# Kernel optimization log

Hardware: AMD Instinct MI355X
Metric: run time of the kernel (lower is better)

The kernel has to match this reference:

```python
import jax, jax.numpy as jnp
import numpy as np
from jax import lax

B, T, D, H, L = 16, 256, 128, 128, 4  # batch, seq, input_size, hidden, num_layers
NUM_CLASSES = 10
EPS = 1e-5


def instancenorm(x):
    # x: [B, T, C]; InstanceNorm1d normalizes over the length dim (T) per (B, C),
    # biased variance, eps=1e-5, no affine.
    m = x.mean(axis=1, keepdims=True)
    v = x.var(axis=1, keepdims=True)
    return (x - m) / jnp.sqrt(v + EPS)


def lstm_stack(x, Wih, Whh, bih, bhh):
    # x: [B, T, I]; Wih/Whh: [L, 4H, I_or_H]; bih/bhh: [L, 4H]. Gate order i,f,g,o.
    batch = x.shape[0]
    hid = Whh.shape[-1]
    out = x
    for l in range(Wih.shape[0]):
        wih, whh, b = Wih[l], Whh[l], bih[l] + bhh[l]
        h0 = jnp.zeros((batch, hid), dtype=x.dtype)
        c0 = jnp.zeros((batch, hid), dtype=x.dtype)
        xs = out.swapaxes(0, 1)  # [T, B, I]

        def step(carry, xt):
            h, c = carry
            g = xt @ wih.T + h @ whh.T + b
            i, f, gg, o = jnp.split(g, 4, axis=-1)
            c_new = jax.nn.sigmoid(f) * c + jax.nn.sigmoid(i) * jnp.tanh(gg)
            h_new = jax.nn.sigmoid(o) * jnp.tanh(c_new)
            return (h_new, c_new), h_new

        _, hs = lax.scan(step, (h0, c0), xs)
        out = hs.swapaxes(0, 1)  # [B, T, H]
    return out


def setup_inputs() -> dict:
    key = jax.random.key(0)
    ks = jax.random.split(key, 16)
    s = 1.0 / np.sqrt(H)
    u = lambda k, shape: jax.random.uniform(k, shape, jnp.float32, -s, s)
    return {
        "x": jax.random.normal(ks[0], (B, T, D), jnp.float32),
        "Wih": u(ks[1], (L, 4 * H, D)),   # input_size == hidden_size so shapes stack
        "Whh": u(ks[2], (L, 4 * H, H)),
        "bih": u(ks[3], (L, 4 * H)),
        "bhh": u(ks[4], (L, 4 * H)),
        "proj_h_w": u(ks[5], (H, H)),
        "proj_h_b": u(ks[6], (H,)),
        "proj_x_w": u(ks[7], (H, D)),
        "proj_x_b": u(ks[8], (H,)),
        "attn_w": u(ks[9], (H,)),
        "fc_w": u(ks[10], (NUM_CLASSES, H)),
        "fc_b": u(ks[11], (NUM_CLASSES,)),
    }


def reference(x, Wih, Whh, bih, bhh, proj_h_w, proj_h_b, proj_x_w, proj_x_b, attn_w, fc_w, fc_b):
    batch, seq_len, input_dim = x.shape
    # normalize(): means/stdev are detached; torch std is unbiased (ddof=1)
    means = lax.stop_gradient(x.mean(axis=(0, 1), keepdims=True))
    stdev = lax.stop_gradient(x.std(axis=(0, 1), ddof=1, keepdims=True) + EPS)
    x = (x - means) / stdev
    x = instancenorm(x)

    lstm_out = lstm_stack(x, Wih, Whh, bih, bhh)   # dropout is identity in eval
    lstm_out = instancenorm(lstm_out)

    ph = lstm_out @ proj_h_w.T + proj_h_b           # [B, T, H]
    px = x @ proj_x_w.T + proj_x_b                  # [B, T, H]
    px = instancenorm(px)

    # additive attention over expanded [B, T, D, H] (values identical across D,
    # matching the original broadcast/expand semantics)
    combined = jnp.tanh(
        jnp.broadcast_to((ph + px)[:, :, None, :], (batch, seq_len, input_dim, ph.shape[-1]))
    )
    logits = jnp.einsum("btdh,h->btd", combined, attn_w)       # [B, T, D]
    alpha = jax.nn.softmax(logits.reshape(batch, -1), axis=1)   # softmax over T*D
    attention_map = alpha.reshape(batch, seq_len, input_dim)

    # classify: context = sum over (T, D) of lstm_out_ex * alpha
    context = jnp.einsum("bth,btd->bh", ph, attention_map)      # [B, H]
    out = context @ fc_w.T + fc_b                               # [B, num_classes]
    return out, attention_map
```

## Files before the change

### kernel.cpp

```cpp
#include <hip/hip_runtime.h>
#include <math.h>
#include <cstddef>

#define B_ 16
#define T_ 256
#define D_ 128
#define H_ 128
#define L_ 4
#define G_ 512
#define NC_ 10
#define EPS_ 1e-5f
#define C_ 16
#define NCHUNK_ (T_ / C_)

#define HROW_ 144
#define HOFF(k) ((k) + (((k) >> 5) << 2))

typedef float f4v __attribute__((ext_vector_type(4)));

#define LOAD_W8(w, base)                                                   \
    asm volatile(                                                          \
        "global_load_dwordx4 %0, %8, off\n\t"                             \
        "global_load_dwordx4 %1, %8, off offset:16\n\t"                   \
        "global_load_dwordx4 %2, %8, off offset:32\n\t"                   \
        "global_load_dwordx4 %3, %8, off offset:48\n\t"                   \
        "global_load_dwordx4 %4, %8, off offset:64\n\t"                   \
        "global_load_dwordx4 %5, %8, off offset:80\n\t"                   \
        "global_load_dwordx4 %6, %8, off offset:96\n\t"                   \
        "global_load_dwordx4 %7, %8, off offset:112\n\t"                  \
        "s_waitcnt vmcnt(0)"                                               \
        : "=&v"(w[0]), "=&v"(w[1]), "=&v"(w[2]), "=&v"(w[3]),              \
          "=&v"(w[4]), "=&v"(w[5]), "=&v"(w[6]), "=&v"(w[7])               \
        : "v"(base)                                                        \
        : "memory")

#define DOT32R(dst_, warr_, hvarr_)                                        \
    {                                                                      \
        float d0_ = 0.f, d1_ = 0.f;                                        \
        _Pragma("unroll")                                                  \
        for (int j_ = 0; j_ < 8; j_++) {                                   \
            d0_ = fmaf(warr_[j_].x, hvarr_[j_].x, d0_);                    \
            d1_ = fmaf(warr_[j_].y, hvarr_[j_].y, d1_);                    \
            d0_ = fmaf(warr_[j_].z, hvarr_[j_].z, d0_);                    \
            d1_ = fmaf(warr_[j_].w, hvarr_[j_].w, d1_);                    \
        }                                                                  \
        dst_ = d0_ + d1_;                                                  \
    }

__device__ __forceinline__ float sigmoid_(float x) {
    x = fminf(fmaxf(x, -30.f), 30.f);
    return 1.f / (1.f + __expf(-x));
}
__device__ __forceinline__ float tanh_(float x) {
    float ax = fminf(fabsf(x), 15.f);
    float e = __expf(2.f * ax);
    float t = 1.f - 2.f / (e + 1.f);
    return copysignf(t, x);
}
__device__ __forceinline__ void wait_ge_(int* p, int v) {
    if (__hip_atomic_load(p, __ATOMIC_RELAXED, __HIP_MEMORY_SCOPE_AGENT) < v) {
        do { __builtin_amdgcn_s_sleep(1); }
        while (__hip_atomic_load(p, __ATOMIC_RELAXED, __HIP_MEMORY_SCOPE_AGENT) < v);
    }
    (void)__hip_atomic_load(p, __ATOMIC_ACQUIRE, __HIP_MEMORY_SCOPE_AGENT);
}
__device__ __forceinline__ void ast_(float* p, float v) {
    __hip_atomic_store(p, v, __ATOMIC_RELAXED, __HIP_MEMORY_SCOPE_AGENT);
}
__device__ __forceinline__ float ald_(const float* p) {
    return __hip_atomic_load(p, __ATOMIC_RELAXED, __HIP_MEMORY_SCOPE_AGENT);
}

__global__ __launch_bounds__(512) void stats_bd(const float* __restrict__ x,
                                                float* __restrict__ psum,
                                                float* __restrict__ psq) {
    int blk = blockIdx.x;
    int b = blk >> 4, strip = blk & 15;
    int tid = threadIdx.x;
    int d = tid & 127, r = tid >> 7;
    const float* xb = x + (size_t)b * T_ * D_ + (size_t)strip * 16 * D_;
    float s = 0.f, q = 0.f;
    for (int t = r; t < 16; t += 4) {
        float v = xb[t * D_ + d];
        s += v; q += v * v;
    }
    __shared__ float ls[512], lq[512];
    ls[tid] = s; lq[tid] = q;
    __syncthreads();
    if (r == 0) {
        s = ls[d] + ls[d + 128] + ls[d + 256] + ls[d + 384];
        q = lq[d] + lq[d + 128] + lq[d + 256] + lq[d + 384];
        psum[blk * 128 + d] = s;
        psq[blk * 128 + d] = q;
    }
}

__global__ __launch_bounds__(128) void stats_norm(const float* __restrict__ psum,
                                                  const float* __restrict__ psq,
                                                  float* __restrict__ mu_bd,
                                                  float* __restrict__ invn) {
    int d = threadIdx.x;
    float S = 0.f, Q = 0.f;
    float sb[16], qb[16];
    for (int b = 0; b < 16; b++) {
        float s = 0.f, q = 0.f;
        for (int st = 0; st < 16; st++) {
            s += psum[(b * 16 + st) * 128 + d];
            q += psq[(b * 16 + st) * 128 + d];
        }
        sb[b] = s; qb[b] = q; S += s; Q += q;
    }
    float n = (float)(B_ * T_);
    float m = S / n;
    float varu = (Q - n * m * m) / (n - 1.f);
    float sd = sqrtf(fmaxf(varu, 0.f)) + EPS_;
    for (int b = 0; b < 16; b++) {
        float mu = sb[b] * (1.f / T_);
        float varT = qb[b] * (1.f / T_) - mu * mu;
        mu_bd[b * 128 + d] = mu;
        invn[b * 128 + d] = rsqrtf(fmaxf(varT, 0.f) + EPS_ * sd * sd);
    }
}

__global__ __attribute__((amdgpu_waves_per_eu(2, 2))) __launch_bounds__(512)
void megascan(const float* __restrict__ x,
              const float* __restrict__ Wih, const float* __restrict__ Whh,
              const float* __restrict__ bih, const float* __restrict__ bhh,
              const float* __restrict__ proj_x_w, const float* __restrict__ proj_x_b,
              const float* __restrict__ proj_h_w, const float* __restrict__ proj_h_b,
              const float* __restrict__ attn_w,
              const float* __restrict__ fc_w, const float* __restrict__ fc_b,
              const float* __restrict__ mu_bd, const float* __restrict__ invn,
              float* __restrict__ h_glob,
              float* __restrict__ ring,
              float* __restrict__ px,
              float* __restrict__ mu_px, float* __restrict__ inv_px,
              float* __restrict__ mu_ln, float* __restrict__ inv_ln,
              float* __restrict__ lsc,
              float* __restrict__ out, float* __restrict__ out_att,
              int* __restrict__ flag_h,
              int* __restrict__ flag_g,
              int* __restrict__ flag_px,
              int* __restrict__ flag_ln,
              int* __restrict__ cnt) {
    const int wg = blockIdx.x;
    const int tid = threadIdx.x;
    __shared__ __align__(16) float shbuf[16 * HROW_];
    __shared__ __align__(16) float sAs[64][32];
    __shared__ __align__(16) float sBs[32][132];
    __shared__ float sred[64][33];
    __shared__ float stmp[256], swsh[256], sctx[512];

    if (wg < 64) {
        const int r = tid >> 2, q = tid & 3;
        const int l = wg >> 4, b = wg & 15;
        f4v w0[8], w1[8], w2[8], w3[8];
        const float* wl = Whh + (size_t)l * G_ * 128;
        LOAD_W8(w0, wl + ((size_t)(0 * 128 + r)) * 128 + q * 32);
        LOAD_W8(w1, wl + ((size_t)(1 * 128 + r)) * 128 + q * 32);
        LOAD_W8(w2, wl + ((size_t)(2 * 128 + r)) * 128 + q * 32);
        LOAD_W8(w3, wl + ((size_t)(3 * 128 + r)) * 128 + q * 32);
        float c = 0.f;
        if (tid < HROW_) shbuf[tid] = 0.f;
        const float* rsl = ring + ((size_t)l * 16 + b) * (4 * C_ * G_);
        float* hob = h_glob + ((size_t)l * 16 + b) * T_ * 128;
        int* fg = flag_g + l * 16 + b;
        int* fh = flag_h + l * 16 + b;
        float hreg[C_];
        __syncthreads();

        for (int k = 0; k < NCHUNK_; k++) {
            if (tid == 0) wait_ge_(fg, k + 1);
            __syncthreads();
#pragma unroll
            for (int half = 0; half < 2; half++) {
                float p0[8], p1[8], p2[8], p3[8];
#pragma unroll
                for (int s8 = 0; s8 < 8; s8++) {
                    int s = half * 8 + s8;
                    const float* gp = rsl + ((size_t)(k & 3) * C_ + s) * G_;
                    p0[s8] = ald_(gp + r);
                    p1[s8] = ald_(gp + 128 + r);
                    p2[s8] = ald_(gp + 256 + r);
                    p3[s8] = ald_(gp + 384 + r);
                }
#pragma unroll
                for (int s8 = 0; s8 < 8; s8++) {
                    int s = half * 8 + s8;
                    int t = k * C_ + s;
                    const f4v* hb4 = (const f4v*)(shbuf + (t & 1) * HROW_ + q * 36);
                    f4v hv[8];
#pragma unroll
                    for (int j = 0; j < 8; j++) hv[j] = hb4[j];
                    float zi, zf, zg, zo;
                    DOT32R(zi, w0, hv);
                    DOT32R(zf, w1, hv);
                    DOT32R(zg, w2, hv);
                    DOT32R(zo, w3, hv);
                    zi += __shfl_xor(zi, 1); zi += __shfl_xor(zi, 2);
                    zf += __shfl_xor(zf, 1); zf += __shfl_xor(zf, 2);
                    zg += __shfl_xor(zg, 1); zg += __shfl_xor(zg, 2);
                    zo += __shfl_xor(zo, 1); zo += __shfl_xor(zo, 2);
                    zi += p0[s8]; zf += p1[s8]; zg += p2[s8]; zo += p3[s8];
                    float ai = sigmoid_(zi), af = sigmoid_(zf);
                    float ag = tanh_(zg),    ao = sigmoid_(zo);
                    c = fmaf(af, c, ai * ag);
                    float hn = ao * tanh_(c);
                    if (q == 0) shbuf[((t + 1) & 1) * HROW_ + HOFF(r)] = hn;
                    hreg[s] = hn;
                    __syncthreads();
                }
            }
            if (q == 0) {
#pragma unroll
                for (int s = 0; s < C_; s++)
                    ast_(hob + (size_t)(k * C_ + s) * 128 + r, hreg[s]);
            }
            __syncthreads();
            if (tid == 0) __hip_atomic_store(fh, k + 1, __ATOMIC_RELEASE, __HIP_MEMORY_SCOPE_AGENT);
        }
    } else if (wg < 128) {
        const int r = tid >> 2, q = tid & 3;
        const int l = (wg - 64) >> 4, b = (wg - 64) & 15;
        f4v w0[8], w1[8], w2[8], w3[8];
        const float* wl = Wih + (size_t)l * G_ * 128;
        LOAD_W8(w0, wl + ((size_t)(0 * 128 + r)) * 128 + q * 32);
        LOAD_W8(w1, wl + ((size_t)(1 * 128 + r)) * 128 + q * 32);
        LOAD_W8(w2, wl + ((size_t)(2 * 128 + r)) * 128 + q * 32);
        LOAD_W8(w3, wl + ((size_t)(3 * 128 + r)) * 128 + q * 32);
        float bs0 = bih[l * G_ + r] + bhh[l * G_ + r];
        float bs1 = bih[l * G_ + 128 + r] + bhh[l * G_ + 128 + r];
        float bs2 = bih[l * G_ + 256 + r] + bhh[l * G_ + 256 + r];
        float bs3 = bih[l * G_ + 384 + r] + bhh[l * G_ + 384 + r];
        const float* hsrc = (l > 0) ? h_glob + ((size_t)(l - 1) * 16 + b) * T_ * 128
                                    : x + (size_t)b * T_ * 128;
        float muk = 0.f, ivk = 1.f;
        if (l == 0) { muk = mu_bd[b * 128 + (tid & 127)]; ivk = invn[b * 128 + (tid & 127)]; }
        float* rout = ring + ((size_t)l * 16 + b) * (4 * C_ * G_);
        int* fhp = (l > 0) ? flag_h + (l - 1) * 16 + b : flag_h;
        int* fhme = flag_h + l * 16 + b;
        int* fgo = flag_g + l * 16 + b;

        for (int k = 0; k < NCHUNK_; k++) {
            if (tid == 0) {
                if (l > 0) wait_ge_(fhp, k + 1);
                if (k >= 4) wait_ge_(fhme, k - 3);
            }
            __syncthreads();
#pragma unroll
            for (int i = 0; i < 4; i++) {
                int idx = i * 512 + tid;
                float v;
                if (l == 0) {
                    v = hsrc[(size_t)k * C_ * 128 + idx];
                    v = (v - muk) * ivk;
                } else {
                    v = ald_(hsrc + (size_t)k * C_ * 128 + idx);
                }
                shbuf[(idx >> 7) * HROW_ + HOFF(idx & 127)] = v;
            }
            __syncthreads();
#pragma unroll
            for (int s = 0; s < C_; s++) {
                const f4v* hb4 = (const f4v*)(shbuf + s * HROW_ + q * 36);
                f4v hv[8];
#pragma unroll
                for (int j = 0; j < 8; j++) hv[j] = hb4[j];
                float z0, z1, z2, z3;
                DOT32R(z0, w0, hv);
                DOT32R(z1, w1, hv);
                DOT32R(z2, w2, hv);
                DOT32R(z3, w3, hv);
                z0 += __shfl_xor(z0, 1); z0 += __shfl_xor(z0, 2);
                z1 += __shfl_xor(z1, 1); z1 += __shfl_xor(z1, 2);
                z2 += __shfl_xor(z2, 1); z2 += __shfl_xor(z2, 2);
                z3 += __shfl_xor(z3, 1); z3 += __shfl_xor(z3, 2);
                if (q == 0) {
                    float* ro = rout + ((size_t)(k & 3) * C_ + s) * G_;
                    ast_(ro + r, z0 + bs0);
                    ast_(ro + 128 + r, z1 + bs1);
                    ast_(ro + 256 + r, z2 + bs2);
                    ast_(ro + 384 + r, z3 + bs3);
                }
            }
            __syncthreads();
            if (tid == 0) __hip_atomic_store(fgo, k + 1, __ATOMIC_RELEASE, __HIP_MEMORY_SCOPE_AGENT);
        }
    } else if (wg < 144) {
        const int b = wg - 128;
        const int h = tid & 127, tq = tid >> 7;
        f4v w0[8], w1[8], w2[8], w3[8];
        LOAD_W8(w0, proj_x_w + (size_t)h * 128 + 0);
        LOAD_W8(w1, proj_x_w + (size_t)h * 128 + 32);
        LOAD_W8(w2, proj_x_w + (size_t)h * 128 + 64);
        LOAD_W8(w3, proj_x_w + (size_t)h * 128 + 96);
        float bsx = proj_x_b[h];
        float muk = mu_bd[b * 128 + h], ivk = invn[b * 128 + h];
        const float* xb = x + (size_t)b * T_ * 128;
        float* pxb = px + (size_t)b * T_ * 128;
        float sacc = 0.f, qacc = 0.f;

        for (int blk = 0; blk < 16; blk++) {
            int t0 = blk * 16;
            __syncthreads();
#pragma unroll
            for (int j = 0; j < 4; j++) {
                int tt = tq * 4 + j;
                float v = xb[(size_t)(t0 + tt) * 128 + h];
                shbuf[tt * HROW_ + HOFF(h)] = (v - muk) * ivk;
            }
            __syncthreads();
#pragma unroll
            for (int j = 0; j < 4; j++) {
                int tt = tq * 4 + j;
                const float* row = shbuf + tt * HROW_;
                f4v hv[8];
                float p0, p1, p2, p3;
                const f4v* r4 = (const f4v*)(row + 0 * 36);
#pragma unroll
                for (int u = 0; u < 8; u++) hv[u] = r4[u];
                DOT32R(p0, w0, hv);
                r4 = (const f4v*)(row + 1 * 36);
#pragma unroll
                for (int u = 0; u < 8; u++) hv[u] = r4[u];
                DOT32R(p1, w1, hv);
                r4 = (const f4v*)(row + 2 * 36);
#pragma unroll
                for (int u = 0; u < 8; u++) hv[u] = r4[u];
                DOT32R(p2, w2, hv);
                r4 = (const f4v*)(row + 3 * 36);
#pragma unroll
                for (int u = 0; u < 8; u++) hv[u] = r4[u];
                DOT32R(p3, w3, hv);
                float val = (p0 + p1) + (p2 + p3) + bsx;
                ast_(pxb + (size_t)(t0 + tt) * 128 + h, val);
                sacc += val; qacc += val * val;
            }
        }
        __syncthreads();
        shbuf[tq * 128 + h] = sacc;
        shbuf[512 + tq * 128 + h] = qacc;
        __syncthreads();
        if (tq == 0) {
            float s = shbuf[h] + shbuf[128 + h] + shbuf[256 + h] + shbuf[384 + h];
            float qq = shbuf[512 + h] + shbuf[640 + h] + shbuf[768 + h] + shbuf[896 + h];
            float m = s * (1.f / T_);
            float v = qq * (1.f / T_) - m * m;
            ast_(mu_px + b * 128 + h, m);
            ast_(inv_px + b * 128 + h, rsqrtf(fmaxf(v, 0.f) + EPS_));
        }
        __syncthreads();
        if (tid == 0) __hip_atomic_store(flag_px + b, 1, __ATOMIC_RELEASE, __HIP_MEMORY_SCOPE_AGENT);
    } else if (wg < 160) {
        const int b = wg - 144;
        const int h = tid & 127, st = tid >> 7;
        const float* hsrc = h_glob + ((size_t)3 * 16 + b) * T_ * 128;
        int* f3 = flag_h + 3 * 16 + b;
        float s = 0.f, q = 0.f;
        for (int k = 0; k < NCHUNK_; k++) {
            if (tid == 0) wait_ge_(f3, k + 1);
            __syncthreads();
#pragma unroll
            for (int j = 0; j < 4; j++) {
                int tt = st * 4 + j;
                float v = ald_(hsrc + (size_t)(k * C_ + tt) * 128 + h);
                s += v; q += v * v;
            }
        }
        shbuf[st * 128 + h] = s;
        shbuf[512 + st * 128 + h] = q;
        __syncthreads();
        if (st == 0) {
            float ss = shbuf[h] + shbuf[128 + h] + shbuf[256 + h] + shbuf[384 + h];
            float qq = shbuf[512 + h] + shbuf[640 + h] + shbuf[768 + h] + shbuf[896 + h];
            float m = ss * (1.f / T_);
            float v = qq * (1.f / T_) - m * m;
            ast_(mu_ln + b * 128 + h, m);
            ast_(inv_ln + b * 128 + h, rsqrtf(fmaxf(v, 0.f) + EPS_));
        }
        __syncthreads();
        if (tid == 0) __hip_atomic_store(flag_ln + b, 1, __ATOMIC_RELEASE, __HIP_MEMORY_SCOPE_AGENT);
    } else {
        const int blk = wg - 160;
        const int b = blk >> 2, qt = blk & 3;
        const int m0 = qt * 64;
        if (tid == 0) { wait_ge_(flag_px + b, 1); wait_ge_(flag_ln + b, 1); }
        __syncthreads();

        const float* h3b = h_glob + ((size_t)3 * 16 + b) * T_ * 128;
        float* phg = h_glob;
        const int lr = tid >> 3, lc = (tid & 7) << 2;
        const int nB = tid >> 2, k0B = (tid & 3) << 3;
        const int tm = (tid >> 5) << 2, tn = (tid & 31) << 2;
        float acc[4][4] = {};
        const float* mup = mu_ln + b * 128;
        const float* ivp = inv_ln + b * 128;
        for (int kb = 0; kb < 128; kb += 32) {
            float4 av = *(const float4*)(h3b + (size_t)(m0 + lr) * 128 + kb + lc);
            float4 m4 = *(const float4*)(mup + kb + lc);
            float4 i4 = *(const float4*)(ivp + kb + lc);
            av.x = (av.x - m4.x) * i4.x; av.y = (av.y - m4.y) * i4.y;
            av.z = (av.z - m4.z) * i4.z; av.w = (av.w - m4.w) * i4.w;
            float4 bv0 = *(const float4*)(proj_h_w + (size_t)nB * 128 + kb + k0B);
            float4 bv1 = *(const float4*)(proj_h_w + (size_t)nB * 128 + kb + k0B + 4);
            __syncthreads();
            *(float4*)&sAs[lr][lc] = av;
            sBs[k0B + 0][nB] = bv0.x; sBs[k0B + 1][nB] = bv0.y;
            sBs[k0B + 2][nB] = bv0.z; sBs[k0B + 3][nB] = bv0.w;
            sBs[k0B + 4][nB] = bv1.x; sBs[k0B + 5][nB] = bv1.y;
            sBs[k0B + 6][nB] = bv1.z; sBs[k0B + 7][nB] = bv1.w;
            __syncthreads();
#pragma unroll
            for (int k4 = 0; k4 < 8; k4++) {
                f4v a4[4];
#pragma unroll
                for (int i = 0; i < 4; i++) a4[i] = *(const f4v*)&sAs[tm + i][k4 * 4];
#pragma unroll
                for (int kk = 0; kk < 4; kk++) {
                    f4v b4 = *(const f4v*)&sBs[k4 * 4 + kk][tn];
#pragma unroll
                    for (int i = 0; i < 4; i++) {
                        acc[i][0] = fmaf(a4[i][kk], b4.x, acc[i][0]);
                        acc[i][1] = fmaf(a4[i][kk], b4.y, acc[i][1]);
                        acc[i][2] = fmaf(a4[i][kk], b4.z, acc[i][2]);
                        acc[i][3] = fmaf(a4[i][kk], b4.w, acc[i][3]);
                    }
                }
            }
        }
        float spart[4];
#pragma unroll
        for (int i = 0; i < 4; i++) {
            int t = m0 + tm + i;
            size_t prow = ((size_t)b * 256 + t) * 128;
            float sp = 0.f;
#pragma unroll
            for (int j = 0; j < 4; j++) {
                int col = tn + j;
                float val = acc[i][j] + proj_h_b[col];
                ast_(phg + prow + col, val);
                float inx = (ald_(px + prow + col) - ald_(mu_px + b * 128 + col))
                            * ald_(inv_px + b * 128 + col);
                sp = fmaf(tanh_(val + inx), attn_w[col], sp);
            }
            spart[i] = sp;
        }
        __syncthreads();
#pragma unroll
        for (int i = 0; i < 4; i++) sred[tm + i][tid & 31] = spart[i];
        __syncthreads();
        if (tid < 64) {
            float s = 0.f;
#pragma unroll
            for (int j = 0; j < 32; j++) s += sred[tid][j];
            ast_(lsc + b * 256 + m0 + tid, s);
        }
        __syncthreads();
        if (tid == 0) {
            (void)__hip_atomic_fetch_add(cnt + b, 1, __ATOMIC_ACQ_REL, __HIP_MEMORY_SCOPE_AGENT);
            wait_ge_(cnt + b, 4);
        }
        __syncthreads();
        float v = 0.f;
        if (tid < 256) { v = ald_(lsc + b * 256 + tid); stmp[tid] = v; }
        __syncthreads();
        for (int off = 128; off > 0; off >>= 1) {
            if (tid < off) stmp[tid] = fmaxf(stmp[tid], stmp[tid + off]);
            __syncthreads();
        }
        float mx = stmp[0];
        __syncthreads();
        float e = (tid < 256) ? __expf(v - mx) : 0.f;
        if (tid < 256) stmp[tid] = e;
        __syncthreads();
        for (int off = 128; off > 0; off >>= 1) {
            if (tid < off) stmp[tid] += stmp[tid + off];
            __syncthreads();
        }
        float tot = stmp[0];
        __syncthreads();
        if (tid < 256) swsh[tid] = e / tot;
        __syncthreads();
        {
            float* ob = out_att + (size_t)b * T_ * D_ + (size_t)m0 * 128;
            const float invD = 1.f / (float)D_;
            for (int i = tid; i < 64 * 128; i += 512)
                ob[i] = swsh[m0 + (i >> 7)] * invD;
        }
        if (qt == 0) {
            int h = tid & 127, st = tid >> 7;
            float a = 0.f;
            for (int tt = st * 64; tt < st * 64 + 64; tt++)
                a = fmaf(phg[((size_t)b * 256 + tt) * 128 + h], swsh[tt], a);
            sctx[st * 128 + h] = a;
            __syncthreads();
            if (tid < 128) sctx[tid] = sctx[tid] + sctx[128 + tid] + sctx[256 + tid] + sctx[384 + tid];
            __syncthreads();
            if (tid < NC_) {
                float s = fc_b[tid];
                const float* fw = fc_w + tid * 128;
                for (int k = 0; k < 128; k++) s = fmaf(sctx[k], fw[k], s);
                out[b * NC_ + tid] = s;
            }
        }
    }
}

extern "C" void kernel_launch(void* const* d_in, const int* in_sizes, int n_in,
                              void* d_out, int out_size, void* d_ws, size_t ws_size,
                              hipStream_t stream) {
    const float* x        = (const float*)d_in[0];
    const float* Wih      = (const float*)d_in[1];
    const float* Whh      = (const float*)d_in[2];
    const float* bih      = (const float*)d_in[3];
    const float* bhh      = (const float*)d_in[4];
    const float* proj_h_w = (const float*)d_in[5];
    const float* proj_h_b = (const float*)d_in[6];
    const float* proj_x_w = (const float*)d_in[7];
    const float* proj_x_b = (const float*)d_in[8];
    const float* attn_w   = (const float*)d_in[9];
    const float* fc_w     = (const float*)d_in[10];
    const float* fc_b     = (const float*)d_in[11];
    float* out = (float*)d_out;

    float* ws = (float*)d_ws;
    const size_t NTD = (size_t)B_ * T_ * D_;
    float* h_glob = ws;
    float* ring   = h_glob + 4 * NTD;
    float* px     = ring + 4 * NTD;
    float* smalls = px + NTD;
    float* psum   = smalls;
    float* psq    = psum + 32768;
    float* mu_bd  = psq + 32768;
    float* invn   = mu_bd + 2048;
    float* mu_ln  = invn + 2048;
    float* inv_ln = mu_ln + 2048;
    float* mu_px  = inv_ln + 2048;
    float* inv_px = mu_px + 2048;
    float* lsc    = inv_px + 2048;
    int*   flags  = (int*)(lsc + 4096);
    int*   flag_h  = flags;
    int*   flag_g  = flags + 64;
    int*   flag_px = flags + 128;
    int*   flag_ln = flags + 144;
    int*   cnt     = flags + 160;

    hipMemsetAsync((void*)flags, 0, 256 * sizeof(int), stream);

    stats_bd<<<256, 512, 0, stream>>>(x, psum, psq);
    stats_norm<<<1, 128, 0, stream>>>(psum, psq, mu_bd, invn);

    megascan<<<224, 512, 0, stream>>>(x, Wih, Whh, bih, bhh,
                                      proj_x_w, proj_x_b, proj_h_w, proj_h_b,
                                      attn_w, fc_w, fc_b,
                                      mu_bd, invn, h_glob, ring, px,
                                      mu_px, inv_px, mu_ln, inv_ln,
                                      lsc, out, out + B_ * NC_,
                                      flag_h, flag_g, flag_px, flag_ln, cnt);
}
```

Baseline: 462.7 us.

## Fold input statistics kernels into megascan as extra workgroups with flag sync

Removes the two separate stats kernels and adds 16 extra workgroups to the persistent megascan kernel. Each computes per-batch sums, then all 16 meet at a grid-wide counter barrier before computing normalization parameters and publishing a per-batch flag. Consumer workgroups spin on that flag instead of relying on kernel boundaries, which saves two launches and their serialization. It also caches the px normalization stats in shared memory and swaps atomic loads for plain vector loads in the attention stage. The cost is that the extra workgroups must all be co-resident, otherwise the spin waits could deadlock.

```diff
diff --git a/kernel.cpp b/kernel.cpp
--- a/kernel.cpp
+++ b/kernel.cpp
@@ -71,57 +71,6 @@
     return __hip_atomic_load(p, __ATOMIC_RELAXED, __HIP_MEMORY_SCOPE_AGENT);
 }
 
-__global__ __launch_bounds__(512) void stats_bd(const float* __restrict__ x,
-                                                float* __restrict__ psum,
-                                                float* __restrict__ psq) {
-    int blk = blockIdx.x;
-    int b = blk >> 4, strip = blk & 15;
-    int tid = threadIdx.x;
-    int d = tid & 127, r = tid >> 7;
-    const float* xb = x + (size_t)b * T_ * D_ + (size_t)strip * 16 * D_;
-    float s = 0.f, q = 0.f;
-    for (int t = r; t < 16; t += 4) {
-        float v = xb[t * D_ + d];
-        s += v; q += v * v;
-    }
-    __shared__ float ls[512], lq[512];
-    ls[tid] = s; lq[tid] = q;
-    __syncthreads();
-    if (r == 0) {
-        s = ls[d] + ls[d + 128] + ls[d + 256] + ls[d + 384];
-        q = lq[d] + lq[d + 128] + lq[d + 256] + lq[d + 384];
-        psum[blk * 128 + d] = s;
-        psq[blk * 128 + d] = q;
-    }
-}
-
-__global__ __launch_bounds__(128) void stats_norm(const float* __restrict__ psum,
-                                                  const float* __restrict__ psq,
-                                                  float* __restrict__ mu_bd,
-                                                  float* __restrict__ invn) {
-    int d = threadIdx.x;
-    float S = 0.f, Q = 0.f;
-    float sb[16], qb[16];
-    for (int b = 0; b < 16; b++) {
-        float s = 0.f, q = 0.f;
-        for (int st = 0; st < 16; st++) {
-            s += psum[(b * 16 + st) * 128 + d];
-            q += psq[(b * 16 + st) * 128 + d];
-        }
-        sb[b] = s; qb[b] = q; S += s; Q += q;
-    }
-    float n = (float)(B_ * T_);
-    float m = S / n;
-    float varu = (Q - n * m * m) / (n - 1.f);
-    float sd = sqrtf(fmaxf(varu, 0.f)) + EPS_;
-    for (int b = 0; b < 16; b++) {
-        float mu = sb[b] * (1.f / T_);
-        float varT = qb[b] * (1.f / T_) - mu * mu;
-        mu_bd[b * 128 + d] = mu;
-        invn[b * 128 + d] = rsqrtf(fmaxf(varT, 0.f) + EPS_ * sd * sd);
-    }
-}
-
 __global__ __attribute__((amdgpu_waves_per_eu(2, 2))) __launch_bounds__(512)
 void megascan(const float* __restrict__ x,
               const float* __restrict__ Wih, const float* __restrict__ Whh,
@@ -130,7 +79,8 @@
               const float* __restrict__ proj_h_w, const float* __restrict__ proj_h_b,
               const float* __restrict__ attn_w,
               const float* __restrict__ fc_w, const float* __restrict__ fc_b,
-              const float* __restrict__ mu_bd, const float* __restrict__ invn,
+              float* __restrict__ mu_bd, float* __restrict__ invn,
+              float* __restrict__ psumB, float* __restrict__ psqB,
               float* __restrict__ h_glob,
               float* __restrict__ ring,
               float* __restrict__ px,
@@ -142,7 +92,9 @@
               int* __restrict__ flag_g,
               int* __restrict__ flag_px,
               int* __restrict__ flag_ln,
-              int* __restrict__ cnt) {
+              int* __restrict__ cnt,
+              int* __restrict__ flag_norm,
+              int* __restrict__ cnt_s) {
     const int wg = blockIdx.x;
     const int tid = threadIdx.x;
     __shared__ __align__(16) float shbuf[16 * HROW_];
@@ -150,6 +102,7 @@
     __shared__ __align__(16) float sBs[32][132];
     __shared__ float sred[64][33];
     __shared__ float stmp[256], swsh[256], sctx[512];
+    __shared__ float smu[128], siv[128];
 
     if (wg < 64) {
         const int r = tid >> 2, q = tid & 3;
@@ -235,7 +188,12 @@
         const float* hsrc = (l > 0) ? h_glob + ((size_t)(l - 1) * 16 + b) * T_ * 128
                                     : x + (size_t)b * T_ * 128;
         float muk = 0.f, ivk = 1.f;
-        if (l == 0) { muk = mu_bd[b * 128 + (tid & 127)]; ivk = invn[b * 128 + (tid & 127)]; }
+        if (l == 0) {
+            if (tid == 0) wait_ge_(flag_norm + b, 1);
+            __syncthreads();
+            muk = mu_bd[b * 128 + (tid & 127)];
+            ivk = invn[b * 128 + (tid & 127)];
+        }
         float* rout = ring + ((size_t)l * 16 + b) * (4 * C_ * G_);
         int* fhp = (l > 0) ? flag_h + (l - 1) * 16 + b : flag_h;
         int* fhme = flag_h + l * 16 + b;
@@ -295,6 +253,8 @@
         LOAD_W8(w2, proj_x_w + (size_t)h * 128 + 64);
         LOAD_W8(w3, proj_x_w + (size_t)h * 128 + 96);
         float bsx = proj_x_b[h];
+        if (tid == 0) wait_ge_(flag_norm + b, 1);
+        __syncthreads();
         float muk = mu_bd[b * 128 + h], ivk = invn[b * 128 + h];
         const float* xb = x + (size_t)b * T_ * 128;
         float* pxb = px + (size_t)b * T_ * 128;
@@ -380,11 +340,16 @@
         }
         __syncthreads();
         if (tid == 0) __hip_atomic_store(flag_ln + b, 1, __ATOMIC_RELEASE, __HIP_MEMORY_SCOPE_AGENT);
-    } else {
+    } else if (wg < 224) {
         const int blk = wg - 160;
         const int b = blk >> 2, qt = blk & 3;
         const int m0 = qt * 64;
         if (tid == 0) { wait_ge_(flag_px + b, 1); wait_ge_(flag_ln + b, 1); }
+        __syncthreads();
+        if (tid < 128) {
+            smu[tid] = mu_px[b * 128 + tid];
+            siv[tid] = inv_px[b * 128 + tid];
+        }
         __syncthreads();
 
         const float* h3b = h_glob + ((size_t)3 * 16 + b) * T_ * 128;
@@ -433,14 +398,14 @@
         for (int i = 0; i < 4; i++) {
             int t = m0 + tm + i;
             size_t prow = ((size_t)b * 256 + t) * 128;
+            f4v pxv = *(const f4v*)(px + prow + tn);
             float sp = 0.f;
 #pragma unroll
             for (int j = 0; j < 4; j++) {
                 int col = tn + j;
                 float val = acc[i][j] + proj_h_b[col];
                 ast_(phg + prow + col, val);
-                float inx = (ald_(px + prow + col) - ald_(mu_px + b * 128 + col))
-                            * ald_(inv_px + b * 128 + col);
+                float inx = (pxv[j] - smu[col]) * siv[col];
                 sp = fmaf(tanh_(val + inx), attn_w[col], sp);
             }
             spart[i] = sp;
@@ -462,7 +427,7 @@
         }
         __syncthreads();
         float v = 0.f;
-        if (tid < 256) { v = ald_(lsc + b * 256 + tid); stmp[tid] = v; }
+        if (tid < 256) { v = lsc[b * 256 + tid]; stmp[tid] = v; }
         __syncthreads();
         for (int off = 128; off > 0; off >>= 1) {
             if (tid < off) stmp[tid] = fmaxf(stmp[tid], stmp[tid + off]);
@@ -503,6 +468,48 @@
                 out[b * NC_ + tid] = s;
             }
         }
+    } else {
+        const int b = wg - 224;
+        const int d = tid & 127, r = tid >> 7;
+        const float* xb = x + (size_t)b * T_ * 128;
+        float s = 0.f, q = 0.f;
+        for (int t = r; t < T_; t += 4) {
+            float v = xb[(size_t)t * 128 + d];
+            s += v; q += v * v;
+        }
+        shbuf[tid] = s; shbuf[512 + tid] = q;
+        __syncthreads();
+        if (r == 0) {
+            s = shbuf[d] + shbuf[128 + d] + shbuf[256 + d] + shbuf[384 + d];
+            q = shbuf[512 + d] + shbuf[640 + d] + shbuf[768 + d] + shbuf[896 + d];
+            ast_(psumB + b * 128 + d, s);
+            ast_(psqB + b * 128 + d, q);
+        }
+        __syncthreads();
+        if (tid == 0) {
+            (void)__hip_atomic_fetch_add(cnt_s, 1, __ATOMIC_ACQ_REL, __HIP_MEMORY_SCOPE_AGENT);
+            wait_ge_(cnt_s, 16);
+        }
+        __syncthreads();
+        if (tid < 128) {
+            float S = 0.f, Q = 0.f, sb = 0.f, qb = 0.f;
+            for (int bb = 0; bb < 16; bb++) {
+                float ps = psumB[bb * 128 + tid];
+                float pq = psqB[bb * 128 + tid];
+                S += ps; Q += pq;
+                if (bb == b) { sb = ps; qb = pq; }
+            }
+            float n = (float)(B_ * T_);
+            float m = S / n;
+            float varu = (Q - n * m * m) / (n - 1.f);
+            float sd = sqrtf(fmaxf(varu, 0.f)) + EPS_;
+            float mu = sb * (1.f / T_);
+            float varT = qb * (1.f / T_) - mu * mu;
+            ast_(mu_bd + b * 128 + tid, mu);
+            ast_(invn + b * 128 + tid, rsqrtf(fmaxf(varT, 0.f) + EPS_ * sd * sd));
+        }
+        __syncthreads();
+        if (tid == 0) __hip_atomic_store(flag_norm + b, 1, __ATOMIC_RELEASE, __HIP_MEMORY_SCOPE_AGENT);
     }
 }
 
@@ -529,9 +536,9 @@
     float* ring   = h_glob + 4 * NTD;
     float* px     = ring + 4 * NTD;
     float* smalls = px + NTD;
-    float* psum   = smalls;
-    float* psq    = psum + 32768;
-    float* mu_bd  = psq + 32768;
+    float* psumB  = smalls;
+    float* psqB   = psumB + 2048;
+    float* mu_bd  = psqB + 2048;
     float* invn   = mu_bd + 2048;
     float* mu_ln  = invn + 2048;
     float* inv_ln = mu_ln + 2048;
@@ -539,22 +546,23 @@
     float* inv_px = mu_px + 2048;
     float* lsc    = inv_px + 2048;
     int*   flags  = (int*)(lsc + 4096);
-    int*   flag_h  = flags;
-    int*   flag_g  = flags + 64;
-    int*   flag_px = flags + 128;
-    int*   flag_ln = flags + 144;
-    int*   cnt     = flags + 160;
+    int*   flag_h   = flags;
+    int*   flag_g   = flags + 64;
+    int*   flag_px  = flags + 128;
+    int*   flag_ln  = flags + 144;
+    int*   cnt      = flags + 160;
+    int*   flag_norm= flags + 176;
+    int*   cnt_s    = flags + 192;
 
     hipMemsetAsync((void*)flags, 0, 256 * sizeof(int), stream);
 
-    stats_bd<<<256, 512, 0, stream>>>(x, psum, psq);
-    stats_norm<<<1, 128, 0, stream>>>(psum, psq, mu_bd, invn);
-
-    megascan<<<224, 512, 0, stream>>>(x, Wih, Whh, bih, bhh,
+    megascan<<<240, 512, 0, stream>>>(x, Wih, Whh, bih, bhh,
                                       proj_x_w, proj_x_b, proj_h_w, proj_h_b,
                                       attn_w, fc_w, fc_b,
-                                      mu_bd, invn, h_glob, ring, px,
+                                      mu_bd, invn, psumB, psqB,
+                                      h_glob, ring, px,
                                       mu_px, inv_px, mu_ln, inv_ln,
                                       lsc, out, out + B_ * NC_,
-                                      flag_h, flag_g, flag_px, flag_ln, cnt);
-}
+                                      flag_h, flag_g, flag_px, flag_ln, cnt,
+                                      flag_norm, cnt_s);
+}
```

Result: faster. 450.2 us (-2.7%).
